# Performance work log

Hardware: AMD Instinct MI355X
Metric: run time of the kernel (lower is better)

## Reference

```python
import jax, jax.numpy as jnp
import numpy as np

B, S, M = 4, 4096, 2048
LATENT, H, D = 512, 16, 128  # latent_dim, num_heads, hidden_dim (per-head)


def setup_inputs() -> dict:
    key = jax.random.key(0)
    ks = jax.random.split(key, 12)
    sd = lambda fan_in: 1.0 / np.sqrt(fan_in)
    return {
        "x": jax.random.normal(ks[0], (B, S, M), dtype=jnp.float32),
        # k path: down-proj to latent, up-proj to H*D (vmapped Dense pair, slice 0)
        "Wd_k": jax.random.normal(ks[1], (M, LATENT), dtype=jnp.float32) * sd(M),
        "bd_k": jnp.zeros((LATENT,), dtype=jnp.float32),
        "Wu_k": jax.random.normal(ks[2], (LATENT, H * D), dtype=jnp.float32) * sd(LATENT),
        "bu_k": jnp.zeros((H * D,), dtype=jnp.float32),
        # v path (slice 1 of the vmapped params)
        "Wd_v": jax.random.normal(ks[3], (M, LATENT), dtype=jnp.float32) * sd(M),
        "bd_v": jnp.zeros((LATENT,), dtype=jnp.float32),
        "Wu_v": jax.random.normal(ks[4], (LATENT, H * D), dtype=jnp.float32) * sd(LATENT),
        "bu_v": jnp.zeros((H * D,), dtype=jnp.float32),
        # q projection
        "Wq": jax.random.normal(ks[5], (M, H * D), dtype=jnp.float32) * sd(M),
        "bq": jnp.zeros((H * D,), dtype=jnp.float32),
        # output projection
        "Wo": jax.random.normal(ks[6], (H * D, M), dtype=jnp.float32) * sd(H * D),
        "bo": jnp.zeros((M,), dtype=jnp.float32),
    }


def reference(x, Wd_k, bd_k, Wu_k, bu_k, Wd_v, bd_v, Wu_v, bu_v, Wq, bq, Wo, bo):
    b, s, m = x.shape
    # low-rank KV: down-project to latent cache, up-project to heads
    cache_k = x @ Wd_k + bd_k                      # [B,S,L]
    cache_v = x @ Wd_v + bd_v                      # [B,S,L]
    k = (cache_k @ Wu_k + bu_k).reshape(b, s, H, D)
    v = (cache_v @ Wu_v + bu_v).reshape(b, s, H, D)
    q = (x @ Wq + bq).reshape(b, s, H, D)
    # NOTE: source permutes k as (0,1,3,2) on [B,S,H,D] -> scores are per-token
    # head-vs-head [B,S,H,H], softmax over the last (head) axis.
    sim = jnp.einsum("bshd,bsgd->bshg", q, k) * (D ** -0.5)
    attn = jax.nn.softmax(sim, axis=-1)            # [B,S,H,H]
    out = jnp.einsum("bshg,bsgd->bshd", attn, v)   # [B,S,H,D]
    out = out.reshape(b, s, H * D)
    return out @ Wo + bo                           # [B,S,M]
```

## Files before the change

### kernel.cpp

```cpp
#include <hip/hip_runtime.h>

typedef __attribute__((ext_vector_type(8))) short short8v;
typedef __attribute__((ext_vector_type(4))) float f32x4;
typedef __attribute__((ext_vector_type(4))) unsigned int uint4v;

#define GLOBAL_AS(p) ((const __attribute__((address_space(1))) void*)(p))
#define LDS_AS(p)    ((__attribute__((address_space(3))) void*)(p))
#define WAITV(n) asm volatile("s_waitcnt vmcnt(" #n ")" ::: "memory")
#define LGKM0()  asm volatile("s_waitcnt lgkmcnt(0)" ::: "memory")
#define BARRIER() __builtin_amdgcn_s_barrier()
#define SCHED0() __builtin_amdgcn_sched_barrier(0)

__device__ __forceinline__ unsigned short f2bf(float f) {
  unsigned int u = __builtin_bit_cast(unsigned int, f);
  u += 0x7fffu + ((u >> 16) & 1u);
  return (unsigned short)(u >> 16);
}
__device__ __forceinline__ float bf2f(unsigned short u) {
  unsigned int x = ((unsigned int)u) << 16;
  return __builtin_bit_cast(float, x);
}

__global__ __launch_bounds__(256) void transpose_to_bf16(
    const float* __restrict__ src, unsigned short* __restrict__ dst,
    int K, int N, int ntx) {
  __shared__ float tile[32][33];
  const int bx = blockIdx.x % ntx;
  const int by = blockIdx.x / ntx;
  const int tx = threadIdx.x & 31, ty = threadIdx.x >> 5;
  const int k0 = by * 32, n0 = bx * 32;
#pragma unroll
  for (int i = 0; i < 32; i += 8)
    tile[ty + i][tx] = src[(size_t)(k0 + ty + i) * N + n0 + tx];
  __syncthreads();
#pragma unroll
  for (int i = 0; i < 32; i += 8)
    dst[(size_t)(n0 + ty + i) * K + k0 + tx] = f2bf(tile[tx][ty + i]);
}

__global__ __launch_bounds__(256) void cvt_f32_bf16(
    const float* __restrict__ s, unsigned short* __restrict__ d) {
  size_t i = ((size_t)blockIdx.x * 256 + threadIdx.x) * 8;
  f32x4 v0 = *(const f32x4*)(s + i);
  f32x4 v1 = *(const f32x4*)(s + i + 4);
  union U8 { uint4v v; unsigned short us[8]; } o;
  o.us[0] = f2bf(v0.x); o.us[1] = f2bf(v0.y); o.us[2] = f2bf(v0.z); o.us[3] = f2bf(v0.w);
  o.us[4] = f2bf(v1.x); o.us[5] = f2bf(v1.y); o.us[6] = f2bf(v1.z); o.us[7] = f2bf(v1.w);
  *(uint4v*)(d + i) = o.v;
}

__global__ __launch_bounds__(256) void fill_bias(
    const float* __restrict__ bd_k, const float* __restrict__ bd_v,
    const float* __restrict__ bq, const float* __restrict__ bu_k,
    const float* __restrict__ bu_v, float* __restrict__ b1, float* __restrict__ b2) {
  int i = blockIdx.x * 256 + threadIdx.x;
  if (i < 512) b1[i] = bd_k[i];
  else if (i < 1024) b1[i] = bd_v[i - 512];
  else if (i < 3072) b1[i] = bq[i - 1024];
  else if (i < 5120) b2[i - 3072] = bu_k[i - 3072];
  else if (i < 7168) b2[i - 3072] = bu_v[i - 5120];
}

template <int OUT_BF16>
__global__ __launch_bounds__(512, 2) void gemm_bt(
    const unsigned short* __restrict__ A, int lda, int nsplit_col, int acol_off,
    const unsigned short* __restrict__ Bt, int ldb,
    const float* __restrict__ bias, void* __restrict__ Cp, int ldc,
    int K, int ntn) {
  __shared__ unsigned short lds[2][2][256 * 64];
  const int t = threadIdx.x;
  const int lane = t & 63, wave = t >> 6;

  const int qx = gridDim.x >> 3;
  const int bid = (blockIdx.x & 7) * qx + (blockIdx.x >> 3);
  const int bm = (bid / ntn) * 256;
  const int bn = (bid % ntn) * 256;
  const unsigned short* Ab = A + (bn >= nsplit_col ? acol_off : 0);

  const int wr = wave >> 2, wc = wave & 3;
  const int g = lane >> 4, r = lane & 15;
  const int swz = r & 7;
  const int NT = K >> 6;

  f32x4 acc[8][4];
#pragma unroll
  for (int i = 0; i < 8; ++i)
#pragma unroll
    for (int j = 0; j < 4; ++j) acc[i][j] = (f32x4){0.f, 0.f, 0.f, 0.f};

  const int trow = t >> 3;
  const int jsrc = (t & 7) ^ (trow & 7);
  const unsigned short* aptr = Ab + (size_t)(bm + trow) * lda + (jsrc << 3);
  const unsigned short* bptr = Bt + (size_t)(bn + trow) * ldb + (jsrc << 3);
  const int wbase = wave * 512;

  auto stageA = [&](int kt, int buf, int q64) {
    __builtin_amdgcn_global_load_lds(
        GLOBAL_AS(aptr + (size_t)(q64 * 64) * lda + kt * 64),
        LDS_AS(&lds[buf][0][q64 * 4096 + wbase]), 16, 0, 0);
  };
  auto stageB = [&](int kt, int buf, int q64) {
    __builtin_amdgcn_global_load_lds(
        GLOBAL_AS(bptr + (size_t)(q64 * 64) * ldb + kt * 64),
        LDS_AS(&lds[buf][1][q64 * 4096 + wbase]), 16, 0, 0);
  };

  auto phaseReads = [&](const unsigned short* la, const unsigned short* lb,
                        int miH, int ks, short8v (&af)[4], short8v (&bf)[4]) {
    const int c16 = (((ks << 2) + g) ^ swz) << 3;
#pragma unroll
    for (int mi = 0; mi < 4; ++mi)
      af[mi] = *(const short8v*)&la[(wr * 128 + miH * 64 + mi * 16 + r) * 64 + c16];
#pragma unroll
    for (int ni = 0; ni < 4; ++ni)
      bf[ni] = *(const short8v*)&lb[(wc * 64 + ni * 16 + r) * 64 + c16];
  };
  auto phaseMfma = [&](int miH, short8v (&af)[4], short8v (&bf)[4]) {
    __builtin_amdgcn_s_setprio(1);
#pragma unroll
    for (int mi = 0; mi < 4; ++mi)
#pragma unroll
      for (int ni = 0; ni < 4; ++ni)
        acc[miH * 4 + mi][ni] = __builtin_amdgcn_mfma_f32_16x16x32_bf16(
            af[mi], bf[ni], acc[miH * 4 + mi][ni], 0, 0, 0);
    __builtin_amdgcn_s_setprio(0);
  };

  stageA(0, 0, 0); stageA(0, 0, 1); stageA(0, 0, 2); stageA(0, 0, 3);
  stageB(0, 0, 0); stageB(0, 0, 1); stageB(0, 0, 2); stageB(0, 0, 3);
  WAITV(0);
  BARRIER();

  for (int T = 0; T < NT; ++T) {
    const int cur = T & 1, nxt = cur ^ 1;
    const unsigned short* la = lds[cur][0];
    const unsigned short* lb = lds[cur][1];
    const bool s1 = (T + 1 < NT);
    short8v af[4], bf[4];

    phaseReads(la, lb, 0, 0, af, bf);
    if (s1) { stageA(T + 1, nxt, 0); stageA(T + 1, nxt, 2); }
    BARRIER();
    LGKM0(); SCHED0();
    phaseMfma(0, af, bf);
    BARRIER();

    phaseReads(la, lb, 0, 1, af, bf);
    if (s1) { stageB(T + 1, nxt, 0); stageB(T + 1, nxt, 1); }
    BARRIER();
    LGKM0(); SCHED0();
    phaseMfma(0, af, bf);
    if (s1) { WAITV(4); } else { WAITV(0); }
    BARRIER();

    phaseReads(la, lb, 1, 0, af, bf);
    if (s1) { stageB(T + 1, nxt, 2); stageB(T + 1, nxt, 3); }
    BARRIER();
    LGKM0(); SCHED0();
    phaseMfma(1, af, bf);
    BARRIER();

    phaseReads(la, lb, 1, 1, af, bf);
    if (s1) { stageA(T + 1, nxt, 1); stageA(T + 1, nxt, 3); }
    BARRIER();
    LGKM0(); SCHED0();
    phaseMfma(1, af, bf);
    if (s1) { WAITV(2); }
    BARRIER();
  }

#pragma unroll
  for (int ni = 0; ni < 4; ++ni) {
    const int col = bn + wc * 64 + ni * 16 + r;
    const float bv = bias[col];
#pragma unroll
    for (int mi = 0; mi < 8; ++mi) {
      const int row0 = bm + wr * 128 + mi * 16 + (g << 2);
#pragma unroll
      for (int j = 0; j < 4; ++j) {
        float v = acc[mi][ni][j] + bv;
        if (OUT_BF16)
          ((unsigned short*)Cp)[(size_t)(row0 + j) * ldc + col] = f2bf(v);
        else
          ((float*)Cp)[(size_t)(row0 + j) * ldc + col] = v;
      }
    }
  }
}

__global__ __launch_bounds__(256) void attn_kernel(
    const unsigned short* __restrict__ out1, const unsigned short* __restrict__ kv,
    unsigned short* __restrict__ aout) {
  const int s = blockIdx.x;
  const int t = threadIdx.x;
  __shared__ float qs[16 * 132], ks2[16 * 132], vs[16 * 132];
  __shared__ float attn[256];
  const int h = t >> 4, d0 = (t & 15) * 8;

  union U8 { uint4v v; unsigned short us[8]; };
  U8 qv, kv8, vv;
  qv.v = *(const uint4v*)(out1 + (size_t)s * 3072 + 1024 + t * 8);
  kv8.v = *(const uint4v*)(kv + (size_t)s * 4096 + t * 8);
  vv.v = *(const uint4v*)(kv + (size_t)s * 4096 + 2048 + t * 8);
#pragma unroll
  for (int j = 0; j < 8; ++j) {
    qs[h * 132 + d0 + j] = bf2f(qv.us[j]);
    ks2[h * 132 + d0 + j] = bf2f(kv8.us[j]);
    vs[h * 132 + d0 + j] = bf2f(vv.us[j]);
  }
  __syncthreads();

  const int gg0 = t & 15;
  const f32x4* qrow = (const f32x4*)&qs[h * 132];
  const f32x4* krow = (const f32x4*)&ks2[gg0 * 132];
  float acc = 0.f;
#pragma unroll
  for (int dd = 0; dd < 32; ++dd) {
    f32x4 a4 = qrow[dd], b4 = krow[dd];
    acc += a4.x * b4.x + a4.y * b4.y + a4.z * b4.z + a4.w * b4.w;
  }
  acc *= 0.08838834764831845f;
  float mx = acc;
#pragma unroll
  for (int o = 8; o; o >>= 1) mx = fmaxf(mx, __shfl_xor(mx, o));
  float e = __expf(acc - mx);
  float sm = e;
#pragma unroll
  for (int o = 8; o; o >>= 1) sm += __shfl_xor(sm, o);
  attn[t] = e / sm;
  __syncthreads();

  f32x4 o0 = (f32x4){0.f, 0.f, 0.f, 0.f}, o1 = (f32x4){0.f, 0.f, 0.f, 0.f};
#pragma unroll
  for (int gg = 0; gg < 16; ++gg) {
    const float a = attn[(h << 4) + gg];
    f32x4 v0 = *(const f32x4*)&vs[gg * 132 + d0];
    f32x4 v1 = *(const f32x4*)&vs[gg * 132 + d0 + 4];
    o0 += v0 * a;
    o1 += v1 * a;
  }
  U8 ov;
  ov.us[0] = f2bf(o0.x); ov.us[1] = f2bf(o0.y); ov.us[2] = f2bf(o0.z); ov.us[3] = f2bf(o0.w);
  ov.us[4] = f2bf(o1.x); ov.us[5] = f2bf(o1.y); ov.us[6] = f2bf(o1.z); ov.us[7] = f2bf(o1.w);
  *(uint4v*)(aout + (size_t)s * 2048 + t * 8) = ov.v;
}

extern "C" void kernel_launch(void* const* d_in, const int* in_sizes, int n_in,
                              void* d_out, int out_size, void* d_ws, size_t ws_size,
                              hipStream_t stream) {
  (void)in_sizes; (void)n_in; (void)out_size; (void)ws_size;
  const float* x    = (const float*)d_in[0];
  const float* Wd_k = (const float*)d_in[1];
  const float* bd_k = (const float*)d_in[2];
  const float* Wu_k = (const float*)d_in[3];
  const float* bu_k = (const float*)d_in[4];
  const float* Wd_v = (const float*)d_in[5];
  const float* bd_v = (const float*)d_in[6];
  const float* Wu_v = (const float*)d_in[7];
  const float* bu_v = (const float*)d_in[8];
  const float* Wq   = (const float*)d_in[9];
  const float* bq   = (const float*)d_in[10];
  const float* Wo   = (const float*)d_in[11];
  const float* bo   = (const float*)d_in[12];

  char* ws = (char*)d_ws;
  unsigned short* w1t  = (unsigned short*)(ws);
  unsigned short* w2t  = (unsigned short*)(ws + 12582912);
  unsigned short* w3t  = (unsigned short*)(ws + 16777216);
  float*          b1   = (float*)(ws + 25165824);
  float*          b2   = (float*)(ws + 25178112);
  unsigned short* xb   = (unsigned short*)(ws + 25194496);
  unsigned short* out1 = (unsigned short*)(ws + 92303360);
  unsigned short* kvb  = (unsigned short*)(ws + 192966656);
  unsigned short* attO = xb;

  dim3 blk(256);

  transpose_to_bf16<<<dim3(16 * 64), blk, 0, stream>>>(Wd_k, w1t,               2048, 512, 16);
  transpose_to_bf16<<<dim3(16 * 64), blk, 0, stream>>>(Wd_v, w1t + 512 * 2048,  2048, 512, 16);
  transpose_to_bf16<<<dim3(64 * 64), blk, 0, stream>>>(Wq,   w1t + 1024 * 2048, 2048, 2048, 64);
  transpose_to_bf16<<<dim3(64 * 16), blk, 0, stream>>>(Wu_k, w2t,               512, 2048, 64);
  transpose_to_bf16<<<dim3(64 * 16), blk, 0, stream>>>(Wu_v, w2t + 2048 * 512,  512, 2048, 64);
  transpose_to_bf16<<<dim3(64 * 64), blk, 0, stream>>>(Wo,   w3t,               2048, 2048, 64);

  fill_bias<<<dim3(28), blk, 0, stream>>>(bd_k, bd_v, bq, bu_k, bu_v, b1, b2);

  cvt_f32_bf16<<<dim3(16384), blk, 0, stream>>>(x, xb);

  gemm_bt<1><<<dim3(64 * 12), dim3(512), 0, stream>>>(
      xb, 2048, 1 << 30, 0, w1t, 2048, b1, out1, 3072, 2048, 12);

  gemm_bt<1><<<dim3(64 * 16), dim3(512), 0, stream>>>(
      out1, 3072, 2048, 512, w2t, 512, b2, kvb, 4096, 512, 16);

  attn_kernel<<<dim3(16384), blk, 0, stream>>>(out1, kvb, attO);

  gemm_bt<0><<<dim3(64 * 8), dim3(512), 0, stream>>>(
      attO, 2048, 1 << 30, 0, w3t, 2048, bo, (float*)d_out, 2048, 2048, 8);
}
```

Baseline: 612.0 us.

## Deepen GEMM prefetch to two tiles ahead and reuse B fragments across halves

```diff
diff --git a/kernel.cpp b/kernel.cpp
--- a/kernel.cpp
+++ b/kernel.cpp
@@ -105,17 +105,19 @@
         LDS_AS(&lds[buf][1][q64 * 4096 + wbase]), 16, 0, 0);
   };
 
-  auto phaseReads = [&](const unsigned short* la, const unsigned short* lb,
-                        int miH, int ks, short8v (&af)[4], short8v (&bf)[4]) {
+  auto readA = [&](const unsigned short* la, int miH, int ks, short8v (&af)[4]) {
     const int c16 = (((ks << 2) + g) ^ swz) << 3;
 #pragma unroll
     for (int mi = 0; mi < 4; ++mi)
       af[mi] = *(const short8v*)&la[(wr * 128 + miH * 64 + mi * 16 + r) * 64 + c16];
+  };
+  auto readB = [&](const unsigned short* lb, int ks, short8v (&bf)[4]) {
+    const int c16 = (((ks << 2) + g) ^ swz) << 3;
 #pragma unroll
     for (int ni = 0; ni < 4; ++ni)
       bf[ni] = *(const short8v*)&lb[(wc * 64 + ni * 16 + r) * 64 + c16];
   };
-  auto phaseMfma = [&](int miH, short8v (&af)[4], short8v (&bf)[4]) {
+  auto mfma8 = [&](int miH, short8v (&af)[4], short8v (&bf)[4]) {
     __builtin_amdgcn_s_setprio(1);
 #pragma unroll
     for (int mi = 0; mi < 4; ++mi)
@@ -126,47 +128,48 @@
     __builtin_amdgcn_s_setprio(0);
   };
 
-  stageA(0, 0, 0); stageA(0, 0, 1); stageA(0, 0, 2); stageA(0, 0, 3);
   stageB(0, 0, 0); stageB(0, 0, 1); stageB(0, 0, 2); stageB(0, 0, 3);
-  WAITV(0);
-  BARRIER();
+  stageA(0, 0, 0); stageA(0, 0, 2);
+  stageA(0, 0, 1); stageA(0, 0, 3);
+  if (NT > 1) {
+    stageB(1, 1, 0); stageB(1, 1, 1); stageB(1, 1, 2); stageB(1, 1, 3);
+    stageA(1, 1, 0); stageA(1, 1, 2);
+  }
 
   for (int T = 0; T < NT; ++T) {
     const int cur = T & 1, nxt = cur ^ 1;
     const unsigned short* la = lds[cur][0];
     const unsigned short* lb = lds[cur][1];
-    const bool s1 = (T + 1 < NT);
-    short8v af[4], bf[4];
-
-    phaseReads(la, lb, 0, 0, af, bf);
-    if (s1) { stageA(T + 1, nxt, 0); stageA(T + 1, nxt, 2); }
-    BARRIER();
+    const bool s1 = (T + 1 < NT), s2 = (T + 2 < NT);
+    short8v af[4], bf0[4], bf1[4];
+
+    if (s1) { WAITV(8); } else { WAITV(2); }
+    BARRIER(); SCHED0();
+    readA(la, 0, 0, af);
+    readB(lb, 0, bf0);
+    if (s1) { stageA(T + 1, nxt, 1); stageA(T + 1, nxt, 3); }
     LGKM0(); SCHED0();
-    phaseMfma(0, af, bf);
-    BARRIER();
-
-    phaseReads(la, lb, 0, 1, af, bf);
-    if (s1) { stageB(T + 1, nxt, 0); stageB(T + 1, nxt, 1); }
-    BARRIER();
+    mfma8(0, af, bf0);
+
+    BARRIER(); SCHED0();
+    readA(la, 0, 1, af);
+    readB(lb, 1, bf1);
     LGKM0(); SCHED0();
-    phaseMfma(0, af, bf);
-    if (s1) { WAITV(4); } else { WAITV(0); }
-    BARRIER();
-
-    phaseReads(la, lb, 1, 0, af, bf);
-    if (s1) { stageB(T + 1, nxt, 2); stageB(T + 1, nxt, 3); }
-    BARRIER();
+    mfma8(0, af, bf1);
+
+    if (s1) { WAITV(8); } else { WAITV(0); }
+    BARRIER(); SCHED0();
+    readA(la, 1, 0, af);
+    if (s2) { stageB(T + 2, cur, 0); stageB(T + 2, cur, 1);
+              stageB(T + 2, cur, 2); stageB(T + 2, cur, 3); }
     LGKM0(); SCHED0();
-    phaseMfma(1, af, bf);
-    BARRIER();
-
-    phaseReads(la, lb, 1, 1, af, bf);
-    if (s1) { stageA(T + 1, nxt, 1); stageA(T + 1, nxt, 3); }
-    BARRIER();
+    mfma8(1, af, bf0);
+
+    BARRIER(); SCHED0();
+    readA(la, 1, 1, af);
+    if (s2) { stageA(T + 2, cur, 0); stageA(T + 2, cur, 2); }
     LGKM0(); SCHED0();
-    phaseMfma(1, af, bf);
-    if (s1) { WAITV(2); }
-    BARRIER();
+    mfma8(1, af, bf1);
   }
 
 #pragma unroll
```

Result: faster. 579.7 us (-5.3%).
